# Optimization experiments

Hardware: AMD Instinct MI355X
Metric: run time of the kernel (lower is better)

The kernel has to match this reference:

```python
import jax, jax.numpy as jnp
import numpy as np

T, D, L, H = 512, 256, 256, 512  # tokens, embed dim, lstm dims, hidden units


def _lstm(x, W, U, b):
    """Keras-style LSTM over x [T, Din] -> hidden states [T, L].
    Gate order i, f, g(cell), o; sigmoid recurrent activations, tanh cell."""
    Ldim = U.shape[0]

    def step(carry, xt):
        h, c = carry
        z = xt @ W + h @ U + b  # [4L]
        i, f, g, o = jnp.split(z, 4)
        i = jax.nn.sigmoid(i)
        f = jax.nn.sigmoid(f)
        g = jnp.tanh(g)
        o = jax.nn.sigmoid(o)
        c = f * c + i * g
        h = o * jnp.tanh(c)
        return (h, c), h

    h0 = jnp.zeros((Ldim,), x.dtype)
    _, hs = jax.lax.scan(step, (h0, h0), x)
    return hs


def setup_inputs() -> dict:
    key = jax.random.key(0)
    ks = jax.random.split(key, 16)

    def p(k, shape):
        # Glorot-like small init
        fan = shape[0] + shape[-1]
        return jax.random.normal(k, shape, jnp.float32) * np.float32(np.sqrt(2.0 / fan))

    return {
        "embeddings": jax.random.normal(ks[0], (1, T, D), jnp.float32),
        "W_f1": p(ks[1], (D, 4 * L)), "U_f1": p(ks[2], (L, 4 * L)), "b_f1": jnp.zeros((4 * L,), jnp.float32),
        "W_b1": p(ks[3], (D, 4 * L)), "U_b1": p(ks[4], (L, 4 * L)), "b_b1": jnp.zeros((4 * L,), jnp.float32),
        "W_f2": p(ks[5], (2 * L, 4 * L)), "U_f2": p(ks[6], (L, 4 * L)), "b_f2": jnp.zeros((4 * L,), jnp.float32),
        "W_b2": p(ks[7], (2 * L, 4 * L)), "U_b2": p(ks[8], (L, 4 * L)), "b_b2": jnp.zeros((4 * L,), jnp.float32),
        "FOH": p(ks[9], (2 * L, H)),
        "FOM": p(ks[10], (2 * L, H)),
        "hidBias": p(ks[11], (1, H)),
        "outLayer": p(ks[12], (H, 1)),
        "outBias": p(ks[13], (1, 1)),
    }


def reference(embeddings, W_f1, U_f1, b_f1, W_b1, U_b1, b_b1,
              W_f2, U_f2, b_f2, W_b2, U_b2, b_b2,
              FOH, FOM, hidBias, outLayer, outBias):
    x = embeddings[0]  # [T, D]
    # --- FirstBiLSTMModule ---
    rf1 = _lstm(x, W_f1, U_f1, b_f1)            # forward LSTM over sequence
    rb1 = _lstm(x[::-1], W_b1, U_b1, b_b1)      # backward LSTM over reversed sequence
    # concatenate_layers: pair forward step i with backward step T-1-i
    v = jnp.concatenate([rf1, rb1[::-1]], axis=-1)  # [T, 2L]
    # --- NextBiLSTMModule ---
    rf2 = _lstm(v, W_f2, U_f2, b_f2)
    rb2 = _lstm(v[::-1], W_b2, U_b2, b_b2)
    hcat = jnp.concatenate([rf2, rb2[::-1]], axis=-1)  # [T, 2L] per-token concat
    # --- ConcatHeadModule.__evaluate (hidden2_units == 0 path) ---
    headfov = hcat @ FOH  # [T, H]
    modfov = hcat @ FOM   # [T, H]
    # pairwise: activation(headfov_i + modfov_j + hidBias) @ outLayer + outBias
    act = jnp.tanh(headfov[:, None, :] + modfov[None, :, :] + hidBias[0])  # [T, T, H]
    scores = jnp.einsum('ijh,ho->ij', act, outLayer) + outBias[0, 0]       # [T, T]
    return scores
```

## Files before the change

### kernel.cpp

```cpp
#include <hip/hip_runtime.h>
#include <hip/hip_bf16.h>


typedef _Float16 h2v __attribute__((ext_vector_type(2)));
typedef unsigned int u32x8 __attribute__((ext_vector_type(8)));

#define BC(x) __builtin_bit_cast(h2v, (x))

__device__ __forceinline__ float fdot2f(h2v a, h2v b, float c) {
#if __has_builtin(__builtin_amdgcn_fdot2)
    return __builtin_amdgcn_fdot2(a, b, c, false);
#else
    return c + (float)a[0] * (float)b[0] + (float)a[1] * (float)b[1];
#endif
}

__global__ __launch_bounds__(256) void prep_u(const float* __restrict__ U,
                                              unsigned int* __restrict__ Uf) {
    int idx = blockIdx.x * 256 + threadIdx.x;
    int k2 = idx >> 10, col = idx & 1023;
    union { _Float16 h[2]; unsigned int u; } p;
    p.h[0] = (_Float16)U[(2 * k2) * 1024 + col];
    p.h[1] = (_Float16)U[(2 * k2 + 1) * 1024 + col];
    Uf[idx] = p.u;
}

__global__ __launch_bounds__(256) void gemm_bias(const float* __restrict__ A,
                                                 const float* __restrict__ B,
                                                 const float* __restrict__ bias,
                                                 float* __restrict__ C,
                                                 int M, int N, int K, int revA) {
    __shared__ float sA[16][65];
    __shared__ float sB[16][65];
    int tid = threadIdx.x;
    int bm = blockIdx.y * 64, bn = blockIdx.x * 64;
    int tx = tid & 15, ty = tid >> 4;
    float acc[4][4] = {};
    for (int k0 = 0; k0 < K; k0 += 16) {
#pragma unroll
        for (int l = 0; l < 4; l++) {
            int flat = tid + 256 * l;
            int ml = flat >> 4, kk = flat & 15;
            int row = bm + ml;
            if (revA) row = M - 1 - row;
            sA[kk][ml] = A[row * K + k0 + kk];
        }
#pragma unroll
        for (int l = 0; l < 4; l++) {
            int flat = tid + 256 * l;
            int kk = flat >> 6, nl = flat & 63;
            sB[kk][nl] = B[(k0 + kk) * N + bn + nl];
        }
        __syncthreads();
#pragma unroll
        for (int kk = 0; kk < 16; kk++) {
            float a[4], b[4];
#pragma unroll
            for (int i = 0; i < 4; i++) a[i] = sA[kk][ty + 16 * i];
#pragma unroll
            for (int j = 0; j < 4; j++) b[j] = sB[kk][tx + 16 * j];
#pragma unroll
            for (int i = 0; i < 4; i++)
#pragma unroll
                for (int j = 0; j < 4; j++) acc[i][j] += a[i] * b[j];
        }
        __syncthreads();
    }
#pragma unroll
    for (int i = 0; i < 4; i++) {
        int r = bm + ty + 16 * i;
#pragma unroll
        for (int j = 0; j < 4; j++) {
            int cidx = bn + tx + 16 * j;
            float bv = bias ? bias[cidx] : 0.f;
            C[r * N + cidx] = acc[i][j] + bv;
        }
    }
}

#define UAq(r) ((r) < 8 ? q0[(r) & 7] : (r) < 16 ? q1[(r) & 7] : \
                (r) < 24 ? q2[(r) & 7] : (r) < 32 ? q3[(r) & 7] : \
                (r) < 40 ? q4[(r) & 7] : (r) < 48 ? q5[(r) & 7] : \
                (r) < 56 ? q6[(r) & 7] : q7[(r) & 7])

__global__ __launch_bounds__(256) void lstm_quad(
        const unsigned int* __restrict__ Ua, const unsigned int* __restrict__ Ub,
        const float* __restrict__ Pa, const float* __restrict__ Pb,
        float* __restrict__ Oa, float* __restrict__ Ob,
        unsigned long long* Hg) {
    int dir = blockIdx.x >> 2;
    int b = blockIdx.x & 3;
    const unsigned int* U = dir ? Ub : Ua;
    const float* P = dir ? Pb : Pa;
    float* O = dir ? Ob : Oa;
    unsigned long long* Hgd = Hg + dir * 256;

    __shared__ unsigned int sU[64 * 256];
    __shared__ __align__(16) unsigned int sH[128];
    __shared__ float sZ[256];
    __shared__ float sG[64];

    int t = threadIdx.x;
    int col = ((t >> 6) << 8) + (b << 6) + (t & 63);

    for (int kp = 0; kp < 64; kp++) sU[kp * 256 + t] = U[kp * 1024 + col];

    u32x8 q0, q1, q2, q3, q4, q5, q6, q7;
#pragma unroll
    for (int j = 0; j < 8; j++) {
        q0[j] = U[(64 + j) * 1024 + col];
        q1[j] = U[(72 + j) * 1024 + col];
        q2[j] = U[(80 + j) * 1024 + col];
        q3[j] = U[(88 + j) * 1024 + col];
        q4[j] = U[(96 + j) * 1024 + col];
        q5[j] = U[(104 + j) * 1024 + col];
        q6[j] = U[(112 + j) * 1024 + col];
        q7[j] = U[(120 + j) * 1024 + col];
    }
    asm volatile(""
                 : "+v"(q0), "+v"(q1), "+v"(q2), "+v"(q3),
                   "+v"(q4), "+v"(q5), "+v"(q6), "+v"(q7));

    if (t < 128) sH[t] = 0u;
    float c = 0.f;
    __syncthreads();

    const uint4* hp4 = (const uint4*)sH;
    float pc = P[col];
    for (int step = 0; step < 512; step++) {
        float pn = pc;
        if (step < 511) pn = P[(step + 1) * 1024 + col];
        float a0 = pc, a1 = 0.f, a2 = 0.f, a3 = 0.f;

#pragma unroll
        for (int cch = 0; cch < 16; cch++) {
            uint4 hc = hp4[cch];
            const unsigned int* su = &sU[(4 * cch) * 256 + t];
            a0 = fdot2f(BC(hc.x), BC(su[0]), a0);
            a1 = fdot2f(BC(hc.y), BC(su[256]), a1);
            a2 = fdot2f(BC(hc.z), BC(su[512]), a2);
            a3 = fdot2f(BC(hc.w), BC(su[768]), a3);
        }
#pragma unroll
        for (int cch = 16; cch < 32; cch++) {
            uint4 hc = hp4[cch];
            const int r0 = 4 * (cch - 16);
            a0 = fdot2f(BC(hc.x), BC(UAq(r0 + 0)), a0);
            a1 = fdot2f(BC(hc.y), BC(UAq(r0 + 1)), a1);
            a2 = fdot2f(BC(hc.z), BC(UAq(r0 + 2)), a2);
            a3 = fdot2f(BC(hc.w), BC(UAq(r0 + 3)), a3);
        }
        sZ[t] = (a0 + a1) + (a2 + a3);
        __syncthreads();

        unsigned long long* Hbuf = Hgd + ((step + 1) & 1) * 128;
        unsigned long long tag = (unsigned long long)(step + 1);
        if (t < 64) {
            float zi = sZ[t], zf = sZ[64 + t], zg = sZ[128 + t], zo = sZ[192 + t];
            float ig = 1.f / (1.f + __expf(-zi));
            float fg = 1.f / (1.f + __expf(-zf));
            float gg = 1.f - 2.f / (1.f + __expf(2.f * zg));
            float og = 1.f / (1.f + __expf(-zo));
            c = fg * c + ig * gg;
            float h = og * (1.f - 2.f / (1.f + __expf(2.f * c)));
            O[step * 256 + (b << 6) + t] = h;
            sG[t] = h;
            if (t < 32) {
                union { _Float16 hh[2]; unsigned int u; } pk;
                pk.hh[0] = (_Float16)sG[2 * t];
                pk.hh[1] = (_Float16)sG[2 * t + 1];
                unsigned long long v = (tag << 32) | (unsigned long long)pk.u;
                __hip_atomic_store(&Hbuf[(b << 5) + t], v, __ATOMIC_RELAXED,
                                   __HIP_MEMORY_SCOPE_AGENT);
            }
        }
        if (t < 128) {
            unsigned long long v;
            do {
                v = __hip_atomic_load(&Hbuf[t], __ATOMIC_RELAXED,
                                      __HIP_MEMORY_SCOPE_AGENT);
            } while ((v >> 32) != tag);
            sH[t] = (unsigned int)v;
        }
        __syncthreads();
        pc = pn;
    }
}

__global__ __launch_bounds__(256) void concat_k(const float* __restrict__ F,
                                                const float* __restrict__ Bk,
                                                float* __restrict__ V) {
    int idx = blockIdx.x * 256 + threadIdx.x;
    int t = idx >> 9, d = idx & 511;
    V[idx] = (d < 256) ? F[t * 256 + d] : Bk[(511 - t) * 256 + d - 256];
}

__global__ __launch_bounds__(256) void head_kernel(const float* __restrict__ HF,
                                                   const float* __restrict__ MF,
                                                   const float* __restrict__ w,
                                                   const float* __restrict__ outb,
                                                   float* __restrict__ S) {
    int i = blockIdx.x;
    __shared__ float sHF[512], sW[512];
    int tid = threadIdx.x;
    sHF[tid] = HF[i * 512 + tid];
    sHF[tid + 256] = HF[i * 512 + 256 + tid];
    sW[tid] = w[tid];
    sW[tid + 256] = w[tid + 256];
    __syncthreads();
    int lane = tid & 63, wv = tid >> 6;
    float ob = outb[0];
    for (int j = wv; j < 512; j += 4) {
        const float* mf = MF + j * 512;
        float acc = 0.f;
#pragma unroll
        for (int r = 0; r < 8; r++) {
            int h = lane + 64 * r;
            float x = sHF[h] + mf[h];
            acc += sW[h] * (1.f - 2.f / (1.f + __expf(2.f * x)));
        }
#pragma unroll
        for (int off = 32; off; off >>= 1) acc += __shfl_down(acc, off);
        if (lane == 0) S[i * 512 + j] = acc + ob;
    }
}

extern "C" void kernel_launch(void* const* d_in, const int* in_sizes, int n_in,
                              void* d_out, int out_size, void* d_ws, size_t ws_size,
                              hipStream_t stream) {
    const float* emb      = (const float*)d_in[0];
    const float* W_f1     = (const float*)d_in[1];
    const float* U_f1     = (const float*)d_in[2];
    const float* b_f1     = (const float*)d_in[3];
    const float* W_b1     = (const float*)d_in[4];
    const float* U_b1     = (const float*)d_in[5];
    const float* b_b1     = (const float*)d_in[6];
    const float* W_f2     = (const float*)d_in[7];
    const float* U_f2     = (const float*)d_in[8];
    const float* b_f2     = (const float*)d_in[9];
    const float* W_b2     = (const float*)d_in[10];
    const float* U_b2     = (const float*)d_in[11];
    const float* b_b2     = (const float*)d_in[12];
    const float* FOH      = (const float*)d_in[13];
    const float* FOM      = (const float*)d_in[14];
    const float* hidBias  = (const float*)d_in[15];
    const float* outLayer = (const float*)d_in[16];
    const float* outBias  = (const float*)d_in[17];
    float* out = (float*)d_out;

    unsigned int* uf = (unsigned int*)d_ws;
    unsigned int* uf_f1 = uf;
    unsigned int* uf_b1 = uf + 131072;
    unsigned int* uf_f2 = uf + 262144;
    unsigned int* uf_b2 = uf + 393216;
    float* f = (float*)d_ws + 524288;
    float* P1f = f;
    float* P1b = f + 524288;
    float* P2f = f + 1048576;
    float* P2b = f + 1572864;
    float* rf1 = f + 2097152;
    float* rb1 = f + 2228224;
    float* rf2 = f + 2359296;
    float* rb2 = f + 2490368;
    float* v    = f + 2621440;
    float* hcat = f + 2883584;
    float* HFb  = f + 3145728;
    float* MFb  = f + 3407872;
    unsigned long long* sync = (unsigned long long*)(f + 3407872);

    prep_u<<<512, 256, 0, stream>>>(U_f1, uf_f1);
    prep_u<<<512, 256, 0, stream>>>(U_b1, uf_b1);
    prep_u<<<512, 256, 0, stream>>>(U_f2, uf_f2);
    prep_u<<<512, 256, 0, stream>>>(U_b2, uf_b2);

    dim3 g1(1024 / 64, 512 / 64);
    gemm_bias<<<g1, 256, 0, stream>>>(emb, W_f1, b_f1, P1f, 512, 1024, 256, 0);
    gemm_bias<<<g1, 256, 0, stream>>>(emb, W_b1, b_b1, P1b, 512, 1024, 256, 1);

    hipMemsetAsync(sync, 0, 4096, stream);
    lstm_quad<<<8, 256, 0, stream>>>(uf_f1, uf_b1, P1f, P1b, rf1, rb1, sync);

    concat_k<<<1024, 256, 0, stream>>>(rf1, rb1, v);

    gemm_bias<<<g1, 256, 0, stream>>>(v, W_f2, b_f2, P2f, 512, 1024, 512, 0);
    gemm_bias<<<g1, 256, 0, stream>>>(v, W_b2, b_b2, P2b, 512, 1024, 512, 1);

    hipMemsetAsync(sync, 0, 4096, stream);
    lstm_quad<<<8, 256, 0, stream>>>(uf_f2, uf_b2, P2f, P2b, rf2, rb2, sync);

    concat_k<<<1024, 256, 0, stream>>>(rf2, rb2, hcat);

    dim3 g2(512 / 64, 512 / 64);
    gemm_bias<<<g2, 256, 0, stream>>>(hcat, FOH, hidBias, HFb, 512, 512, 512, 0);
    gemm_bias<<<g2, 256, 0, stream>>>(hcat, FOM, nullptr, MFb, 512, 512, 512, 0);

    head_kernel<<<512, 256, 0, stream>>>(HFb, MFb, outLayer, outBias, out);
}
```

Before: 2.467 ms.

## Split LSTM recurrence across two blocks per direction with overlapped exchange

```diff
diff --git a/kernel.cpp b/kernel.cpp
--- a/kernel.cpp
+++ b/kernel.cpp
@@ -83,27 +83,46 @@
                 (r) < 40 ? q4[(r) & 7] : (r) < 48 ? q5[(r) & 7] : \
                 (r) < 56 ? q6[(r) & 7] : q7[(r) & 7])
 
-__global__ __launch_bounds__(256) void lstm_quad(
+#define DOTS_LDS(accA, accB)                                   \
+    _Pragma("unroll") for (int cch = 0; cch < 16; cch++) {     \
+        uint4 hc = hp4[cch];                                   \
+        const unsigned int* su = &sU[(4 * cch) * 512 + t];     \
+        accA = fdot2f(BC(hc.x), BC(su[0]), accA);              \
+        accB = fdot2f(BC(hc.y), BC(su[512]), accB);            \
+        accA = fdot2f(BC(hc.z), BC(su[1024]), accA);           \
+        accB = fdot2f(BC(hc.w), BC(su[1536]), accB);           \
+    }
+
+#define DOTS_REG(accA, accB)                                   \
+    _Pragma("unroll") for (int cch = 16; cch < 32; cch++) {    \
+        uint4 hc = hp4[cch];                                   \
+        const int r0 = 4 * (cch - 16);                         \
+        accA = fdot2f(BC(hc.x), BC(UAq(r0 + 0)), accA);        \
+        accB = fdot2f(BC(hc.y), BC(UAq(r0 + 1)), accB);        \
+        accA = fdot2f(BC(hc.z), BC(UAq(r0 + 2)), accA);        \
+        accB = fdot2f(BC(hc.w), BC(UAq(r0 + 3)), accB);        \
+    }
+
+__global__ __launch_bounds__(512) void lstm_duo(
         const unsigned int* __restrict__ Ua, const unsigned int* __restrict__ Ub,
         const float* __restrict__ Pa, const float* __restrict__ Pb,
         float* __restrict__ Oa, float* __restrict__ Ob,
         unsigned long long* Hg) {
-    int dir = blockIdx.x >> 2;
-    int b = blockIdx.x & 3;
+    int dir = blockIdx.x >> 1;
+    int b = blockIdx.x & 1;
     const unsigned int* U = dir ? Ub : Ua;
     const float* P = dir ? Pb : Pa;
     float* O = dir ? Ob : Oa;
     unsigned long long* Hgd = Hg + dir * 256;
 
-    __shared__ unsigned int sU[64 * 256];
+    __shared__ unsigned int sU[64 * 512];
     __shared__ __align__(16) unsigned int sH[128];
-    __shared__ float sZ[256];
-    __shared__ float sG[64];
+    __shared__ float sZ[512];
 
     int t = threadIdx.x;
-    int col = ((t >> 6) << 8) + (b << 6) + (t & 63);
-
-    for (int kp = 0; kp < 64; kp++) sU[kp * 256 + t] = U[kp * 1024 + col];
+    int col = ((t >> 7) << 8) + (b << 7) + (t & 127);
+
+    for (int kp = 0; kp < 64; kp++) sU[kp * 512 + t] = U[kp * 1024 + col];
 
     u32x8 q0, q1, q2, q3, q4, q5, q6, q7;
 #pragma unroll
@@ -122,7 +141,7 @@
                    "+v"(q4), "+v"(q5), "+v"(q6), "+v"(q7));
 
     if (t < 128) sH[t] = 0u;
-    float c = 0.f;
+    float c0 = 0.f, c1 = 0.f;
     __syncthreads();
 
     const uint4* hp4 = (const uint4*)sH;
@@ -130,57 +149,62 @@
     for (int step = 0; step < 512; step++) {
         float pn = pc;
         if (step < 511) pn = P[(step + 1) * 1024 + col];
-        float a0 = pc, a1 = 0.f, a2 = 0.f, a3 = 0.f;
-
-#pragma unroll
-        for (int cch = 0; cch < 16; cch++) {
-            uint4 hc = hp4[cch];
-            const unsigned int* su = &sU[(4 * cch) * 256 + t];
-            a0 = fdot2f(BC(hc.x), BC(su[0]), a0);
-            a1 = fdot2f(BC(hc.y), BC(su[256]), a1);
-            a2 = fdot2f(BC(hc.z), BC(su[512]), a2);
-            a3 = fdot2f(BC(hc.w), BC(su[768]), a3);
-        }
-#pragma unroll
-        for (int cch = 16; cch < 32; cch++) {
-            uint4 hc = hp4[cch];
-            const int r0 = 4 * (cch - 16);
-            a0 = fdot2f(BC(hc.x), BC(UAq(r0 + 0)), a0);
-            a1 = fdot2f(BC(hc.y), BC(UAq(r0 + 1)), a1);
-            a2 = fdot2f(BC(hc.z), BC(UAq(r0 + 2)), a2);
-            a3 = fdot2f(BC(hc.w), BC(UAq(r0 + 3)), a3);
-        }
+
+        unsigned long long* rslot = nullptr;
+        unsigned long long rv = 0;
+        if (t >= 64 && t < 128) {
+            rslot = &Hgd[(step & 1) * 128 + (1 - b) * 64 + (t - 64)];
+            rv = __hip_atomic_load(rslot, __ATOMIC_RELAXED,
+                                   __HIP_MEMORY_SCOPE_AGENT);
+        }
+
+        float a0 = pc, a1 = 0.f;
+        if (b == 0) { DOTS_LDS(a0, a1) } else { DOTS_REG(a0, a1) }
+
+        if (t >= 64 && t < 128) {
+            unsigned long long v = rv;
+            unsigned long long want = (unsigned long long)step;
+            while ((v >> 32) != want) {
+                __builtin_amdgcn_s_sleep(1);
+                v = __hip_atomic_load(rslot, __ATOMIC_RELAXED,
+                                      __HIP_MEMORY_SCOPE_AGENT);
+            }
+            sH[(1 - b) * 64 + (t - 64)] = (unsigned int)v;
+        }
+        __syncthreads();
+
+        float a2 = 0.f, a3 = 0.f;
+        if (b == 0) { DOTS_REG(a2, a3) } else { DOTS_LDS(a2, a3) }
+
         sZ[t] = (a0 + a1) + (a2 + a3);
         __syncthreads();
 
-        unsigned long long* Hbuf = Hgd + ((step + 1) & 1) * 128;
-        unsigned long long tag = (unsigned long long)(step + 1);
         if (t < 64) {
-            float zi = sZ[t], zf = sZ[64 + t], zg = sZ[128 + t], zo = sZ[192 + t];
-            float ig = 1.f / (1.f + __expf(-zi));
-            float fg = 1.f / (1.f + __expf(-zf));
-            float gg = 1.f - 2.f / (1.f + __expf(2.f * zg));
-            float og = 1.f / (1.f + __expf(-zo));
-            c = fg * c + ig * gg;
-            float h = og * (1.f - 2.f / (1.f + __expf(2.f * c)));
-            O[step * 256 + (b << 6) + t] = h;
-            sG[t] = h;
-            if (t < 32) {
-                union { _Float16 hh[2]; unsigned int u; } pk;
-                pk.hh[0] = (_Float16)sG[2 * t];
-                pk.hh[1] = (_Float16)sG[2 * t + 1];
-                unsigned long long v = (tag << 32) | (unsigned long long)pk.u;
-                __hip_atomic_store(&Hbuf[(b << 5) + t], v, __ATOMIC_RELAXED,
-                                   __HIP_MEMORY_SCOPE_AGENT);
-            }
-        }
-        if (t < 128) {
-            unsigned long long v;
-            do {
-                v = __hip_atomic_load(&Hbuf[t], __ATOMIC_RELAXED,
-                                      __HIP_MEMORY_SCOPE_AGENT);
-            } while ((v >> 32) != tag);
-            sH[t] = (unsigned int)v;
+            float2 z0 = ((const float2*)sZ)[t];
+            float2 z1 = ((const float2*)(sZ + 128))[t];
+            float2 z2 = ((const float2*)(sZ + 256))[t];
+            float2 z3 = ((const float2*)(sZ + 384))[t];
+            float ig0 = 1.f / (1.f + __expf(-z0.x));
+            float fg0 = 1.f / (1.f + __expf(-z1.x));
+            float gg0 = 1.f - 2.f / (1.f + __expf(2.f * z2.x));
+            float og0 = 1.f / (1.f + __expf(-z3.x));
+            c0 = fg0 * c0 + ig0 * gg0;
+            float h0 = og0 * (1.f - 2.f / (1.f + __expf(2.f * c0)));
+            float ig1 = 1.f / (1.f + __expf(-z0.y));
+            float fg1 = 1.f / (1.f + __expf(-z1.y));
+            float gg1 = 1.f - 2.f / (1.f + __expf(2.f * z2.y));
+            float og1 = 1.f / (1.f + __expf(-z3.y));
+            c1 = fg1 * c1 + ig1 * gg1;
+            float h1 = og1 * (1.f - 2.f / (1.f + __expf(2.f * c1)));
+            union { _Float16 hh[2]; unsigned int u; } pk;
+            pk.hh[0] = (_Float16)h0;
+            pk.hh[1] = (_Float16)h1;
+            unsigned long long v =
+                ((unsigned long long)(step + 1) << 32) | (unsigned long long)pk.u;
+            __hip_atomic_store(&Hgd[((step + 1) & 1) * 128 + (b << 6) + t], v,
+                               __ATOMIC_RELAXED, __HIP_MEMORY_SCOPE_AGENT);
+            ((float2*)(O + step * 256 + (b << 7)))[t] = make_float2(h0, h1);
+            sH[(b << 6) + t] = pk.u;
         }
         __syncthreads();
         pc = pn;
@@ -278,7 +302,7 @@
     gemm_bias<<<g1, 256, 0, stream>>>(emb, W_b1, b_b1, P1b, 512, 1024, 256, 1);
 
     hipMemsetAsync(sync, 0, 4096, stream);
-    lstm_quad<<<8, 256, 0, stream>>>(uf_f1, uf_b1, P1f, P1b, rf1, rb1, sync);
+    lstm_duo<<<4, 512, 0, stream>>>(uf_f1, uf_b1, P1f, P1b, rf1, rb1, sync);
 
     concat_k<<<1024, 256, 0, stream>>>(rf1, rb1, v);
 
@@ -286,7 +310,7 @@
     gemm_bias<<<g1, 256, 0, stream>>>(v, W_b2, b_b2, P2b, 512, 1024, 512, 1);
 
     hipMemsetAsync(sync, 0, 4096, stream);
-    lstm_quad<<<8, 256, 0, stream>>>(uf_f2, uf_b2, P2f, P2b, rf2, rb2, sync);
+    lstm_duo<<<4, 512, 0, stream>>>(uf_f2, uf_b2, P2f, P2b, rf2, rb2, sync);
 
     concat_k<<<1024, 256, 0, stream>>>(rf2, rb2, hcat);
 
```

New measurement: 2.526 ms. +2.4%, slower.

## Batch launches, write LSTM outputs directly into concatenated layout, vectorize GEMM

Applied to the files above, without the earlier changes.

```diff
diff --git a/kernel.cpp b/kernel.cpp
--- a/kernel.cpp
+++ b/kernel.cpp
@@ -15,23 +15,36 @@
 #endif
 }
 
-__global__ __launch_bounds__(256) void prep_u(const float* __restrict__ U,
-                                              unsigned int* __restrict__ Uf) {
-    int idx = blockIdx.x * 256 + threadIdx.x;
+__global__ __launch_bounds__(256) void prep_u4(const float* __restrict__ U0,
+                                               const float* __restrict__ U1,
+                                               const float* __restrict__ U2,
+                                               const float* __restrict__ U3,
+                                               unsigned int* __restrict__ Uf) {
+    int g = blockIdx.x >> 9;
+    int idx = (blockIdx.x & 511) * 256 + threadIdx.x;
+    const float* U = (g == 0) ? U0 : (g == 1) ? U1 : (g == 2) ? U2 : U3;
     int k2 = idx >> 10, col = idx & 1023;
     union { _Float16 h[2]; unsigned int u; } p;
     p.h[0] = (_Float16)U[(2 * k2) * 1024 + col];
     p.h[1] = (_Float16)U[(2 * k2 + 1) * 1024 + col];
-    Uf[idx] = p.u;
-}
-
-__global__ __launch_bounds__(256) void gemm_bias(const float* __restrict__ A,
-                                                 const float* __restrict__ B,
-                                                 const float* __restrict__ bias,
-                                                 float* __restrict__ C,
-                                                 int M, int N, int K, int revA) {
-    __shared__ float sA[16][65];
-    __shared__ float sB[16][65];
+    Uf[g * 131072 + idx] = p.u;
+}
+
+__global__ __launch_bounds__(256) void gemm2(const float* __restrict__ A,
+                                             const float* __restrict__ B0,
+                                             const float* __restrict__ B1,
+                                             const float* __restrict__ bias0,
+                                             const float* __restrict__ bias1,
+                                             float* __restrict__ C0,
+                                             float* __restrict__ C1,
+                                             int M, int N, int K, int rev1) {
+    const float* B = blockIdx.z ? B1 : B0;
+    const float* bias = blockIdx.z ? bias1 : bias0;
+    float* C = blockIdx.z ? C1 : C0;
+    int revA = blockIdx.z ? rev1 : 0;
+
+    __shared__ __align__(16) float sA[16][68];
+    __shared__ __align__(16) float sB[16][68];
     int tid = threadIdx.x;
     int bm = blockIdx.y * 64, bn = blockIdx.x * 64;
     int tx = tid & 15, ty = tid >> 4;
@@ -54,11 +67,10 @@
         __syncthreads();
 #pragma unroll
         for (int kk = 0; kk < 16; kk++) {
-            float a[4], b[4];
-#pragma unroll
-            for (int i = 0; i < 4; i++) a[i] = sA[kk][ty + 16 * i];
-#pragma unroll
-            for (int j = 0; j < 4; j++) b[j] = sB[kk][tx + 16 * j];
+            float4 av = *(const float4*)&sA[kk][4 * ty];
+            float4 bv = *(const float4*)&sB[kk][4 * tx];
+            float a[4] = {av.x, av.y, av.z, av.w};
+            float b[4] = {bv.x, bv.y, bv.z, bv.w};
 #pragma unroll
             for (int i = 0; i < 4; i++)
 #pragma unroll
@@ -66,15 +78,14 @@
         }
         __syncthreads();
     }
+    float4 bb = make_float4(0.f, 0.f, 0.f, 0.f);
+    if (bias) bb = *(const float4*)&bias[bn + 4 * tx];
 #pragma unroll
     for (int i = 0; i < 4; i++) {
-        int r = bm + ty + 16 * i;
-#pragma unroll
-        for (int j = 0; j < 4; j++) {
-            int cidx = bn + tx + 16 * j;
-            float bv = bias ? bias[cidx] : 0.f;
-            C[r * N + cidx] = acc[i][j] + bv;
-        }
+        int r = bm + 4 * ty + i;
+        float4 cv = make_float4(acc[i][0] + bb.x, acc[i][1] + bb.y,
+                                acc[i][2] + bb.z, acc[i][3] + bb.w);
+        *(float4*)&C[r * N + bn + 4 * tx] = cv;
     }
 }
 
@@ -86,13 +97,11 @@
 __global__ __launch_bounds__(256) void lstm_quad(
         const unsigned int* __restrict__ Ua, const unsigned int* __restrict__ Ub,
         const float* __restrict__ Pa, const float* __restrict__ Pb,
-        float* __restrict__ Oa, float* __restrict__ Ob,
-        unsigned long long* Hg) {
+        float* __restrict__ Ov, unsigned long long* Hg) {
     int dir = blockIdx.x >> 2;
     int b = blockIdx.x & 3;
     const unsigned int* U = dir ? Ub : Ua;
     const float* P = dir ? Pb : Pa;
-    float* O = dir ? Ob : Oa;
     unsigned long long* Hgd = Hg + dir * 256;
 
     __shared__ unsigned int sU[64 * 256];
@@ -163,7 +172,8 @@
             float og = 1.f / (1.f + __expf(-zo));
             c = fg * c + ig * gg;
             float h = og * (1.f - 2.f / (1.f + __expf(2.f * c)));
-            O[step * 256 + (b << 6) + t] = h;
+            int orow = dir ? (511 - step) : step;
+            Ov[orow * 512 + (dir << 8) + (b << 6) + t] = h;
             sG[t] = h;
             if (t < 32) {
                 union { _Float16 hh[2]; unsigned int u; } pk;
@@ -185,14 +195,6 @@
         __syncthreads();
         pc = pn;
     }
-}
-
-__global__ __launch_bounds__(256) void concat_k(const float* __restrict__ F,
-                                                const float* __restrict__ Bk,
-                                                float* __restrict__ V) {
-    int idx = blockIdx.x * 256 + threadIdx.x;
-    int t = idx >> 9, d = idx & 511;
-    V[idx] = (d < 256) ? F[t * 256 + d] : Bk[(511 - t) * 256 + d - 256];
 }
 
 __global__ __launch_bounds__(256) void head_kernel(const float* __restrict__ HF,
@@ -258,41 +260,30 @@
     float* P1b = f + 524288;
     float* P2f = f + 1048576;
     float* P2b = f + 1572864;
-    float* rf1 = f + 2097152;
-    float* rb1 = f + 2228224;
-    float* rf2 = f + 2359296;
-    float* rb2 = f + 2490368;
     float* v    = f + 2621440;
     float* hcat = f + 2883584;
     float* HFb  = f + 3145728;
     float* MFb  = f + 3407872;
     unsigned long long* sync = (unsigned long long*)(f + 3407872);
 
-    prep_u<<<512, 256, 0, stream>>>(U_f1, uf_f1);
-    prep_u<<<512, 256, 0, stream>>>(U_b1, uf_b1);
-    prep_u<<<512, 256, 0, stream>>>(U_f2, uf_f2);
-    prep_u<<<512, 256, 0, stream>>>(U_b2, uf_b2);
-
-    dim3 g1(1024 / 64, 512 / 64);
-    gemm_bias<<<g1, 256, 0, stream>>>(emb, W_f1, b_f1, P1f, 512, 1024, 256, 0);
-    gemm_bias<<<g1, 256, 0, stream>>>(emb, W_b1, b_b1, P1b, 512, 1024, 256, 1);
+    prep_u4<<<2048, 256, 0, stream>>>(U_f1, U_b1, U_f2, U_b2, uf);
+
+    dim3 g1(1024 / 64, 512 / 64, 2);
+    gemm2<<<g1, 256, 0, stream>>>(emb, W_f1, W_b1, b_f1, b_b1, P1f, P1b,
+                                  512, 1024, 256, 1);
 
     hipMemsetAsync(sync, 0, 4096, stream);
-    lstm_quad<<<8, 256, 0, stream>>>(uf_f1, uf_b1, P1f, P1b, rf1, rb1, sync);
-
-    concat_k<<<1024, 256, 0, stream>>>(rf1, rb1, v);
-
-    gemm_bias<<<g1, 256, 0, stream>>>(v, W_f2, b_f2, P2f, 512, 1024, 512, 0);
-    gemm_bias<<<g1, 256, 0, stream>>>(v, W_b2, b_b2, P2b, 512, 1024, 512, 1);
+    lstm_quad<<<8, 256, 0, stream>>>(uf_f1, uf_b1, P1f, P1b, v, sync);
+
+    gemm2<<<g1, 256, 0, stream>>>(v, W_f2, W_b2, b_f2, b_b2, P2f, P2b,
+                                  512, 1024, 512, 1);
 
     hipMemsetAsync(sync, 0, 4096, stream);
-    lstm_quad<<<8, 256, 0, stream>>>(uf_f2, uf_b2, P2f, P2b, rf2, rb2, sync);
-
-    concat_k<<<1024, 256, 0, stream>>>(rf2, rb2, hcat);
-
-    dim3 g2(512 / 64, 512 / 64);
-    gemm_bias<<<g2, 256, 0, stream>>>(hcat, FOH, hidBias, HFb, 512, 512, 512, 0);
-    gemm_bias<<<g2, 256, 0, stream>>>(hcat, FOM, nullptr, MFb, 512, 512, 512, 0);
+    lstm_quad<<<8, 256, 0, stream>>>(uf_f2, uf_b2, P2f, P2b, hcat, sync);
+
+    dim3 g2(512 / 64, 512 / 64, 2);
+    gemm2<<<g2, 256, 0, stream>>>(hcat, FOH, FOM, hidBias, nullptr, HFb, MFb,
+                                  512, 512, 512, 0);
 
     head_kernel<<<512, 256, 0, stream>>>(HFb, MFb, outLayer, outBias, out);
 }
```

After: 2.260 ms (median of 2 runs). -8.4%, faster.
